# Kernel optimization log

Hardware: AMD Instinct MI355X
Metric: run time of the kernel (lower is better)

The kernel has to match this reference:

```python
import jax, jax.numpy as jnp
import numpy as np

D_MODEL = 1024
NHEAD = 16
D_HEAD = D_MODEL // NHEAD


def setup_inputs() -> dict:
    key = jax.random.key(0)
    ks = jax.random.split(key, 11)
    B, S = 4, 1024
    s = 1.0 / np.sqrt(D_MODEL)
    inp = {
        'q_in': jax.random.normal(ks[0], (B, S, D_MODEL), jnp.float32),
        'k_in': jax.random.normal(ks[1], (B, S, D_MODEL), jnp.float32),
        'v_in': jax.random.normal(ks[2], (B, S, D_MODEL), jnp.float32),
        'Wq': jax.random.normal(ks[3], (D_MODEL, D_MODEL), jnp.float32) * s,
        'bq': jnp.zeros((D_MODEL,), jnp.float32),
        'Wk': jax.random.normal(ks[4], (D_MODEL, D_MODEL), jnp.float32) * s,
        'bk': jnp.zeros((D_MODEL,), jnp.float32),
        'Wv': jax.random.normal(ks[5], (D_MODEL, D_MODEL), jnp.float32) * s,
        'bv': jnp.zeros((D_MODEL,), jnp.float32),
        'Wo': jax.random.normal(ks[6], (D_MODEL, D_MODEL), jnp.float32) * s,
        'bo': jnp.zeros((D_MODEL,), jnp.float32),
    }
    return inp


def reference(q_in, k_in, v_in, Wq, bq, Wk, bk, Wv, bv, Wo, bo):
    B, Sq, _ = q_in.shape
    Sk = k_in.shape[1]
    # Linear projections (torch Linear: x @ W.T + b; here W stored as [in, out])
    Q = q_in @ Wq + bq
    K = k_in @ Wk + bk
    V = v_in @ Wv + bv
    # [B, H, S, Dh]
    Qh = Q.reshape(B, Sq, NHEAD, D_HEAD).transpose(0, 2, 1, 3)
    Kh = K.reshape(B, Sk, NHEAD, D_HEAD).transpose(0, 2, 1, 3)
    Vh = V.reshape(B, Sk, NHEAD, D_HEAD).transpose(0, 2, 1, 3)
    scores = jnp.einsum('bhqd,bhkd->bhqk', Qh, Kh) / jnp.sqrt(jnp.float32(D_HEAD))
    attn_weights = jax.nn.softmax(scores, axis=-1)
    attn = jnp.einsum('bhqk,bhkd->bhqd', attn_weights, Vh)
    attn = attn.transpose(0, 2, 1, 3).reshape(B, Sq, D_MODEL)
    out = attn @ Wo + bo
    return out
```

## Files before the change

### kernel.cpp

```cpp
#include <hip/hip_runtime.h>
#include <hip/hip_bf16.h>
#include <cstdint>
#include <cstddef>

typedef __bf16 bf16_t;
typedef __bf16 bf16x8 __attribute__((ext_vector_type(8)));
typedef __bf16 bf16x4 __attribute__((ext_vector_type(4)));
typedef float f32x4 __attribute__((ext_vector_type(4)));

#define DM 1024
#define NHEAD 16
#define DHEAD 64

#define QSCALE 0.18033688011112042f
#define PSHIFT 4.0f
#define RS 72

__device__ __forceinline__ void gload_lds16(const void* g, void* l) {
    __builtin_amdgcn_global_load_lds(
        (const __attribute__((address_space(1))) void*)g,
        (__attribute__((address_space(3))) void*)l,
        16, 0, 0);
}

__device__ __forceinline__ uint4 cvt8(float4 lo, float4 hi) {
    union { bf16_t b[8]; uint4 u; } o;
    o.b[0] = (bf16_t)lo.x; o.b[1] = (bf16_t)lo.y; o.b[2] = (bf16_t)lo.z; o.b[3] = (bf16_t)lo.w;
    o.b[4] = (bf16_t)hi.x; o.b[5] = (bf16_t)hi.y; o.b[6] = (bf16_t)hi.z; o.b[7] = (bf16_t)hi.w;
    return o.u;
}

__global__ void prep(
    const float* __restrict__ q_in, const float* __restrict__ k_in, const float* __restrict__ v_in,
    bf16_t* __restrict__ Xq, bf16_t* __restrict__ Xk, bf16_t* __restrict__ Xv,
    const float* __restrict__ w0, const float* __restrict__ w1,
    const float* __restrict__ w2, const float* __restrict__ w3,
    bf16_t* __restrict__ t0, bf16_t* __restrict__ t1,
    bf16_t* __restrict__ t2, bf16_t* __restrict__ t3)
{
    __shared__ float tile[32][33];
    int id = blockIdx.x;
    if (id < 6144) {
        int plane = id >> 11;
        int blk = id & 2047;
        const float* x = plane == 0 ? q_in : plane == 1 ? k_in : v_in;
        bf16_t* y      = plane == 0 ? Xq   : plane == 1 ? Xk   : Xv;
        int i = (blk * 256 + threadIdx.x) * 8;
        float4 lo = *(const float4*)&x[i];
        float4 hi = *(const float4*)&x[i + 4];
        *(uint4*)&y[i] = cvt8(lo, hi);
    } else {
        int t = id - 6144;
        int zi = t >> 10;
        int blk = t & 1023;
        const float* w = zi == 0 ? w0 : zi == 1 ? w1 : zi == 2 ? w2 : w3;
        bf16_t* wt     = zi == 0 ? t0 : zi == 1 ? t1 : zi == 2 ? t2 : t3;
        int bx = (blk & 31) * 32;
        int by = (blk >> 5) * 32;
        int tx = threadIdx.x & 31, ty = threadIdx.x >> 5;
        for (int j = 0; j < 32; j += 8)
            tile[ty + j][tx] = w[(size_t)(by + ty + j) * DM + bx + tx];
        __syncthreads();
        for (int j = 0; j < 32; j += 8)
            wt[(size_t)(bx + ty + j) * DM + by + tx] = (bf16_t)tile[tx][ty + j];
    }
}

template <int MODE>
__device__ __forceinline__ void gemm_body(
    const bf16_t* __restrict__ A, const bf16_t* __restrict__ Bt,
    const float* __restrict__ bias, float scale,
    float* __restrict__ Cf, bf16_t* __restrict__ Cb,
    int r0, int c0, bf16_t* AsP, bf16_t* BsP)
{
    const int K = 1024;
    int tid  = threadIdx.x;
    int wave = tid >> 6;
    int lane = tid & 63;
    int quad = lane >> 4;
    int ln   = lane & 15;
    int wr   = wave >> 1;
    int wc   = wave & 1;

    f32x4 acc[4][4];
    for (int rb = 0; rb < 4; rb++)
        for (int cb = 0; cb < 4; cb++)
            acc[rb][cb] = (f32x4){0.f, 0.f, 0.f, 0.f};

    int sr = tid >> 2;
    int sk = (tid & 3) * 8;

    const bf16_t* gA0 = &A[(size_t)(r0 + sr) * K + sk];
    const bf16_t* gA1 = gA0 + (size_t)64 * K;
    const bf16_t* gB0 = &Bt[(size_t)(c0 + sr) * K + sk];
    const bf16_t* gB1 = gB0 + (size_t)64 * K;
    char* lA = (char*)AsP + wave * 1024;
    char* lB = (char*)BsP + wave * 1024;

    for (int k0 = 0; k0 < K; k0 += 32) {
        __syncthreads();
        gload_lds16(gA0 + k0, lA);
        gload_lds16(gA1 + k0, lA + 4096);
        gload_lds16(gB0 + k0, lB);
        gload_lds16(gB1 + k0, lB + 4096);
        __syncthreads();

        bf16x8 af[4], bfv[4];
        for (int rb = 0; rb < 4; rb++)
            af[rb] = *(const bf16x8*)&AsP[(wr * 64 + rb * 16 + ln) * 32 + quad * 8];
        for (int cb = 0; cb < 4; cb++)
            bfv[cb] = *(const bf16x8*)&BsP[(wc * 64 + cb * 16 + ln) * 32 + quad * 8];
        for (int rb = 0; rb < 4; rb++)
            for (int cb = 0; cb < 4; cb++)
                acc[rb][cb] = __builtin_amdgcn_mfma_f32_16x16x32_bf16(af[rb], bfv[cb], acc[rb][cb], 0, 0, 0);
    }

    for (int rb = 0; rb < 4; rb++) {
        for (int cb = 0; cb < 4; cb++) {
            int C = c0 + wc * 64 + cb * 16 + ln;
            for (int r = 0; r < 4; r++) {
                int R = r0 + wr * 64 + rb * 16 + quad * 4 + r;
                float v = acc[rb][cb][r];
                if (MODE == 0) {
                    Cf[(size_t)R * DM + C] = v + bias[C];
                } else if (MODE == 1) {
                    int b = R >> 10, s = R & 1023;
                    int h = C >> 6,  d = C & 63;
                    Cb[(((size_t)b * NHEAD + h) * 1024 + s) * DHEAD + d] =
                        (bf16_t)((v + bias[C]) * scale);
                } else {
                    Cb[((size_t)(C >> 10) * 1024 + R) * 1024 + (C & 1023)] =
                        (bf16_t)(v + bias[R]);
                }
            }
        }
    }
}

__global__ __launch_bounds__(256) void gemm_qkv(
    const bf16_t* __restrict__ Xq, const bf16_t* __restrict__ Xk, const bf16_t* __restrict__ Xv,
    const bf16_t* __restrict__ Wtq, const bf16_t* __restrict__ Wtk, const bf16_t* __restrict__ Wtv,
    const float* __restrict__ bq, const float* __restrict__ bk, const float* __restrict__ bv,
    bf16_t* __restrict__ Qd, bf16_t* __restrict__ Kd, bf16_t* __restrict__ Vt)
{
    __shared__ __align__(16) bf16_t As[128 * 32];
    __shared__ __align__(16) bf16_t Bs[128 * 32];
    int z = blockIdx.z;
    if (z == 0) {
        gemm_body<1>(Xq, Wtq, bq, QSCALE, nullptr, Qd,
                     blockIdx.x * 128, blockIdx.y * 128, As, Bs);
    } else if (z == 1) {
        gemm_body<1>(Xk, Wtk, bk, 1.0f, nullptr, Kd,
                     blockIdx.x * 128, blockIdx.y * 128, As, Bs);
    } else {
        gemm_body<2>(Wtv, Xv, bv, 1.0f, nullptr, Vt,
                     blockIdx.y * 128, blockIdx.x * 128, As, Bs);
    }
}

__global__ __launch_bounds__(256) void gemm_out(
    const bf16_t* __restrict__ At, const bf16_t* __restrict__ Wto,
    const float* __restrict__ bo, float* __restrict__ out)
{
    const int K = 1024;
    __shared__ __align__(16) bf16_t As[64 * 32];
    __shared__ __align__(16) bf16_t Bs[128 * 32];

    int tid  = threadIdx.x;
    int wave = tid >> 6;
    int lane = tid & 63;
    int quad = lane >> 4;
    int ln   = lane & 15;

    int r0 = blockIdx.x * 64;
    int c0 = blockIdx.y * 128;

    f32x4 acc[4][2];
    for (int rb = 0; rb < 4; rb++)
        for (int cb = 0; cb < 2; cb++)
            acc[rb][cb] = (f32x4){0.f, 0.f, 0.f, 0.f};

    int sr = tid >> 2;
    int sk = (tid & 3) * 8;

    const bf16_t* gA0 = At  + (size_t)(r0 + sr) * K + sk;
    const bf16_t* gB0 = Wto + (size_t)(c0 + sr) * K + sk;
    const bf16_t* gB1 = gB0 + (size_t)64 * K;
    char* lA = (char*)As + wave * 1024;
    char* lB = (char*)Bs + wave * 1024;

    for (int k0 = 0; k0 < K; k0 += 32) {
        __syncthreads();
        gload_lds16(gA0 + k0, lA);
        gload_lds16(gB0 + k0, lB);
        gload_lds16(gB1 + k0, lB + 4096);
        __syncthreads();

        bf16x8 af[4], bfv[2];
        for (int rb = 0; rb < 4; rb++)
            af[rb] = *(const bf16x8*)&As[(rb * 16 + ln) * 32 + quad * 8];
        for (int cb = 0; cb < 2; cb++)
            bfv[cb] = *(const bf16x8*)&Bs[(wave * 32 + cb * 16 + ln) * 32 + quad * 8];
        for (int rb = 0; rb < 4; rb++)
            for (int cb = 0; cb < 2; cb++)
                acc[rb][cb] = __builtin_amdgcn_mfma_f32_16x16x32_bf16(af[rb], bfv[cb], acc[rb][cb], 0, 0, 0);
    }

    for (int rb = 0; rb < 4; rb++) {
        for (int cb = 0; cb < 2; cb++) {
            int C = c0 + wave * 32 + cb * 16 + ln;
            float bn = bo[C];
            for (int r = 0; r < 4; r++) {
                int R = r0 + rb * 16 + quad * 4 + r;
                out[(size_t)R * DM + C] = acc[rb][cb][r] + bn;
            }
        }
    }
}

__global__ __launch_bounds__(256) void attn5(
    const bf16_t* __restrict__ Q,
    const bf16_t* __restrict__ K,
    const bf16_t* __restrict__ Vt,
    bf16_t* __restrict__ O)
{
    __shared__ __align__(16) bf16_t Ks[64 * RS];
    __shared__ __align__(16) bf16_t Vs[64 * RS];
    __shared__ __align__(16) bf16_t Ps[4][16 * RS];

    int tid  = threadIdx.x;
    int wave = tid >> 6;
    int lane = tid & 63;
    int quad = lane >> 4;
    int ln   = lane & 15;

    int bh = blockIdx.x;
    int q0w = blockIdx.y * 64 + wave * 16;

    const bf16_t* Qb = Q  + (size_t)bh * 65536;
    const bf16_t* Kb = K  + (size_t)bh * 65536;
    const bf16_t* Vb = Vt + (size_t)bh * 65536;

    int srow = tid >> 3;
    int scol = (tid & 7) * 8;
    const bf16_t* gK0 = Kb + (size_t)srow * 64 + scol;
    const bf16_t* gK1 = gK0 + 32 * 64;
    const bf16_t* gV0 = Vb + (size_t)srow * 1024 + scol;
    const bf16_t* gV1 = gV0 + 32 * 1024;

    bf16x8 aq0 = *(const bf16x8*)&Qb[(size_t)(q0w + ln) * 64 + quad * 8];
    bf16x8 aq1 = *(const bf16x8*)&Qb[(size_t)(q0w + ln) * 64 + 32 + quad * 8];

    uint4 rK0 = *(const uint4*)gK0;
    uint4 rK1 = *(const uint4*)gK1;
    uint4 rV0 = *(const uint4*)gV0;
    uint4 rV1 = *(const uint4*)gV1;

    float l_lane = 0.f;
    f32x4 o_acc[4];
    for (int cb = 0; cb < 4; cb++) o_acc[cb] = (f32x4){0.f, 0.f, 0.f, 0.f};

    bf16_t* Pw = Ps[wave];

    for (int kt = 0; kt < 16; kt++) {
        __syncthreads();
        *(uint4*)&Ks[srow * RS + scol]        = rK0;
        *(uint4*)&Ks[(32 + srow) * RS + scol] = rK1;
        *(uint4*)&Vs[srow * RS + scol]        = rV0;
        *(uint4*)&Vs[(32 + srow) * RS + scol] = rV1;
        __syncthreads();

        if (kt < 15) {
            gK0 += 4096; gK1 += 4096; gV0 += 64; gV1 += 64;
            rK0 = *(const uint4*)gK0;
            rK1 = *(const uint4*)gK1;
            rV0 = *(const uint4*)gV0;
            rV1 = *(const uint4*)gV1;
        }

        f32x4 sc[4];
        for (int kb = 0; kb < 4; kb++) {
            bf16x8 kf0 = *(const bf16x8*)&Ks[(kb * 16 + ln) * RS + quad * 8];
            bf16x8 kf1 = *(const bf16x8*)&Ks[(kb * 16 + ln) * RS + 32 + quad * 8];
            f32x4 a = (f32x4){0.f, 0.f, 0.f, 0.f};
            a = __builtin_amdgcn_mfma_f32_16x16x32_bf16(kf0, aq0, a, 0, 0, 0);
            a = __builtin_amdgcn_mfma_f32_16x16x32_bf16(kf1, aq1, a, 0, 0, 0);
            sc[kb] = a;
        }

        for (int kb = 0; kb < 4; kb++) {
            float p0 = __builtin_amdgcn_exp2f(sc[kb][0] - PSHIFT);
            float p1 = __builtin_amdgcn_exp2f(sc[kb][1] - PSHIFT);
            float p2 = __builtin_amdgcn_exp2f(sc[kb][2] - PSHIFT);
            float p3 = __builtin_amdgcn_exp2f(sc[kb][3] - PSHIFT);
            l_lane += (p0 + p1) + (p2 + p3);
            bf16x4 pk = (bf16x4){(bf16_t)p0, (bf16_t)p1, (bf16_t)p2, (bf16_t)p3};
            *(bf16x4*)&Pw[ln * RS + kb * 16 + quad * 4] = pk;
        }

        for (int kc = 0; kc < 2; kc++) {
            bf16x8 ap = *(const bf16x8*)&Pw[ln * RS + kc * 32 + quad * 8];
            for (int cb = 0; cb < 4; cb++) {
                bf16x8 vf = *(const bf16x8*)&Vs[(cb * 16 + ln) * RS + kc * 32 + quad * 8];
                o_acc[cb] = __builtin_amdgcn_mfma_f32_16x16x32_bf16(ap, vf, o_acc[cb], 0, 0, 0);
            }
        }
    }

    float l = l_lane;
    l += __shfl_xor(l, 16);
    l += __shfl_xor(l, 32);
    float invq[4];
    for (int r = 0; r < 4; r++)
        invq[r] = 1.f / __shfl(l, quad * 4 + r);

    int b = bh >> 4, h = bh & 15;
    for (int cb = 0; cb < 4; cb++) {
        for (int r = 0; r < 4; r++) {
            int q = q0w + quad * 4 + r;
            int d = cb * 16 + ln;
            O[((size_t)b * 1024 + q) * DM + h * 64 + d] = (bf16_t)(o_acc[cb][r] * invq[r]);
        }
    }
}

extern "C" void kernel_launch(void* const* d_in, const int* in_sizes, int n_in,
                              void* d_out, int out_size, void* d_ws, size_t ws_size,
                              hipStream_t stream) {
    const float* q_in = (const float*)d_in[0];
    const float* k_in = (const float*)d_in[1];
    const float* v_in = (const float*)d_in[2];
    const float* Wq   = (const float*)d_in[3];
    const float* bq   = (const float*)d_in[4];
    const float* Wk   = (const float*)d_in[5];
    const float* bk   = (const float*)d_in[6];
    const float* Wv   = (const float*)d_in[7];
    const float* bv   = (const float*)d_in[8];
    const float* Wo   = (const float*)d_in[9];
    const float* bo   = (const float*)d_in[10];

    char* ws = (char*)d_ws;
    const size_t MB = 1024ull * 1024ull;
    bf16_t* Xq  = (bf16_t*)(ws);
    bf16_t* Xk  = (bf16_t*)(ws + 8 * MB);
    bf16_t* Xv  = (bf16_t*)(ws + 16 * MB);
    bf16_t* Wtq = (bf16_t*)(ws + 24 * MB);
    bf16_t* Wtk = (bf16_t*)(ws + 26 * MB);
    bf16_t* Wtv = (bf16_t*)(ws + 28 * MB);
    bf16_t* Wto = (bf16_t*)(ws + 30 * MB);
    bf16_t* Qd  = (bf16_t*)(ws + 32 * MB);
    bf16_t* Kd  = (bf16_t*)(ws + 40 * MB);
    bf16_t* Vt  = (bf16_t*)(ws + 48 * MB);
    bf16_t* At  = Xq;

    prep<<<10240, 256, 0, stream>>>(q_in, k_in, v_in, Xq, Xk, Xv,
                                    Wq, Wk, Wv, Wo, Wtq, Wtk, Wtv, Wto);

    gemm_qkv<<<dim3(32, 8, 3), 256, 0, stream>>>(Xq, Xk, Xv,
                                                 Wtq, Wtk, Wtv, bq, bk, bv, Qd, Kd, Vt);

    attn5<<<dim3(64, 16), 256, 0, stream>>>(Qd, Kd, Vt, At);

    gemm_out<<<dim3(64, 8), 256, 0, stream>>>(At, Wto, bo, (float*)d_out);
}
```

Before: 214.6 us.

## Restructure attention to split keys across waves and reuse shared GEMM body for output

The attention kernel now has each wave own 16 keys of the 64-key tile and compute scores for all 64 queries. K and V tiles are loaded with direct global-to-LDS loads, P is shared through LDS, and row sums are reduced across waves at the end. This drops the register-staged K/V prefetch and per-wave redundant K reads, but adds a third barrier per tile and loses the overlap of the next tile's loads with compute. The output projection now reuses the 128x128 gemm_body tile instead of a dedicated 64x128 kernel, halving the grid.

```diff
diff --git a/kernel.cpp b/kernel.cpp
--- a/kernel.cpp
+++ b/kernel.cpp
@@ -162,162 +162,111 @@
     const bf16_t* __restrict__ At, const bf16_t* __restrict__ Wto,
     const float* __restrict__ bo, float* __restrict__ out)
 {
-    const int K = 1024;
-    __shared__ __align__(16) bf16_t As[64 * 32];
+    __shared__ __align__(16) bf16_t As[128 * 32];
     __shared__ __align__(16) bf16_t Bs[128 * 32];
-
-    int tid  = threadIdx.x;
-    int wave = tid >> 6;
-    int lane = tid & 63;
-    int quad = lane >> 4;
-    int ln   = lane & 15;
-
-    int r0 = blockIdx.x * 64;
-    int c0 = blockIdx.y * 128;
-
-    f32x4 acc[4][2];
-    for (int rb = 0; rb < 4; rb++)
-        for (int cb = 0; cb < 2; cb++)
-            acc[rb][cb] = (f32x4){0.f, 0.f, 0.f, 0.f};
-
-    int sr = tid >> 2;
-    int sk = (tid & 3) * 8;
-
-    const bf16_t* gA0 = At  + (size_t)(r0 + sr) * K + sk;
-    const bf16_t* gB0 = Wto + (size_t)(c0 + sr) * K + sk;
-    const bf16_t* gB1 = gB0 + (size_t)64 * K;
-    char* lA = (char*)As + wave * 1024;
-    char* lB = (char*)Bs + wave * 1024;
-
-    for (int k0 = 0; k0 < K; k0 += 32) {
-        __syncthreads();
-        gload_lds16(gA0 + k0, lA);
-        gload_lds16(gB0 + k0, lB);
-        gload_lds16(gB1 + k0, lB + 4096);
-        __syncthreads();
-
-        bf16x8 af[4], bfv[2];
-        for (int rb = 0; rb < 4; rb++)
-            af[rb] = *(const bf16x8*)&As[(rb * 16 + ln) * 32 + quad * 8];
-        for (int cb = 0; cb < 2; cb++)
-            bfv[cb] = *(const bf16x8*)&Bs[(wave * 32 + cb * 16 + ln) * 32 + quad * 8];
-        for (int rb = 0; rb < 4; rb++)
-            for (int cb = 0; cb < 2; cb++)
-                acc[rb][cb] = __builtin_amdgcn_mfma_f32_16x16x32_bf16(af[rb], bfv[cb], acc[rb][cb], 0, 0, 0);
-    }
-
-    for (int rb = 0; rb < 4; rb++) {
-        for (int cb = 0; cb < 2; cb++) {
-            int C = c0 + wave * 32 + cb * 16 + ln;
-            float bn = bo[C];
-            for (int r = 0; r < 4; r++) {
-                int R = r0 + rb * 16 + quad * 4 + r;
-                out[(size_t)R * DM + C] = acc[rb][cb][r] + bn;
-            }
-        }
-    }
-}
-
-__global__ __launch_bounds__(256) void attn5(
+    gemm_body<0>(At, Wto, bo, 1.0f, out, nullptr,
+                 blockIdx.x * 128, blockIdx.y * 128, As, Bs);
+}
+
+__global__ __launch_bounds__(256) void attn6(
     const bf16_t* __restrict__ Q,
     const bf16_t* __restrict__ K,
     const bf16_t* __restrict__ Vt,
     bf16_t* __restrict__ O)
 {
-    __shared__ __align__(16) bf16_t Ks[64 * RS];
-    __shared__ __align__(16) bf16_t Vs[64 * RS];
-    __shared__ __align__(16) bf16_t Ps[4][16 * RS];
+    __shared__ __align__(16) bf16_t Kp[2][64 * 32];
+    __shared__ __align__(16) bf16_t Vp[2][64 * 32];
+    __shared__ __align__(16) bf16_t Ps[64 * RS];
+    __shared__ float Ls[4][64];
 
     int tid  = threadIdx.x;
-    int wave = tid >> 6;
+    int w    = tid >> 6;
     int lane = tid & 63;
     int quad = lane >> 4;
     int ln   = lane & 15;
 
-    int bh = blockIdx.x;
-    int q0w = blockIdx.y * 64 + wave * 16;
+    int bh  = blockIdx.x;
+    int q0b = blockIdx.y * 64;
 
     const bf16_t* Qb = Q  + (size_t)bh * 65536;
     const bf16_t* Kb = K  + (size_t)bh * 65536;
     const bf16_t* Vb = Vt + (size_t)bh * 65536;
 
-    int srow = tid >> 3;
-    int scol = (tid & 7) * 8;
-    const bf16_t* gK0 = Kb + (size_t)srow * 64 + scol;
-    const bf16_t* gK1 = gK0 + 32 * 64;
-    const bf16_t* gV0 = Vb + (size_t)srow * 1024 + scol;
-    const bf16_t* gV1 = gV0 + 32 * 1024;
-
-    bf16x8 aq0 = *(const bf16x8*)&Qb[(size_t)(q0w + ln) * 64 + quad * 8];
-    bf16x8 aq1 = *(const bf16x8*)&Qb[(size_t)(q0w + ln) * 64 + 32 + quad * 8];
-
-    uint4 rK0 = *(const uint4*)gK0;
-    uint4 rK1 = *(const uint4*)gK1;
-    uint4 rV0 = *(const uint4*)gV0;
-    uint4 rV1 = *(const uint4*)gV1;
-
-    float l_lane = 0.f;
+    bf16x8 aq[4][2];
+    for (int st = 0; st < 4; st++)
+        for (int kc = 0; kc < 2; kc++)
+            aq[st][kc] = *(const bf16x8*)&Qb[(size_t)(q0b + st * 16 + ln) * 64 + kc * 32 + quad * 8];
+
+    int gr = w * 16 + (lane >> 2);
+    int gc = (lane & 3) * 8;
+    char* dK0 = (char*)&Kp[0][0] + w * 1024;
+    char* dK1 = (char*)&Kp[1][0] + w * 1024;
+    char* dV0 = (char*)&Vp[0][0] + w * 1024;
+    char* dV1 = (char*)&Vp[1][0] + w * 1024;
+    const bf16_t* srcV0 = Vb + (size_t)gr * 1024 + gc;
+    const bf16_t* srcV1 = srcV0 + 32;
+
+    float l_acc[4] = {0.f, 0.f, 0.f, 0.f};
     f32x4 o_acc[4];
     for (int cb = 0; cb < 4; cb++) o_acc[cb] = (f32x4){0.f, 0.f, 0.f, 0.f};
 
-    bf16_t* Pw = Ps[wave];
-
     for (int kt = 0; kt < 16; kt++) {
         __syncthreads();
-        *(uint4*)&Ks[srow * RS + scol]        = rK0;
-        *(uint4*)&Ks[(32 + srow) * RS + scol] = rK1;
-        *(uint4*)&Vs[srow * RS + scol]        = rV0;
-        *(uint4*)&Vs[(32 + srow) * RS + scol] = rV1;
-        __syncthreads();
-
-        if (kt < 15) {
-            gK0 += 4096; gK1 += 4096; gV0 += 64; gV1 += 64;
-            rK0 = *(const uint4*)gK0;
-            rK1 = *(const uint4*)gK1;
-            rV0 = *(const uint4*)gV0;
-            rV1 = *(const uint4*)gV1;
-        }
-
+        const bf16_t* kbase = Kb + (size_t)kt * 4096 + (size_t)gr * 64 + gc;
+        gload_lds16(kbase,          dK0);
+        gload_lds16(kbase + 32,     dK1);
+        gload_lds16(srcV0 + kt * 64, dV0);
+        gload_lds16(srcV1 + kt * 64, dV1);
+        __syncthreads();
+
+        bf16x8 kf0 = *(const bf16x8*)&Kp[0][(w * 16 + ln) * 32 + quad * 8];
+        bf16x8 kf1 = *(const bf16x8*)&Kp[1][(w * 16 + ln) * 32 + quad * 8];
         f32x4 sc[4];
-        for (int kb = 0; kb < 4; kb++) {
-            bf16x8 kf0 = *(const bf16x8*)&Ks[(kb * 16 + ln) * RS + quad * 8];
-            bf16x8 kf1 = *(const bf16x8*)&Ks[(kb * 16 + ln) * RS + 32 + quad * 8];
+        for (int st = 0; st < 4; st++) {
             f32x4 a = (f32x4){0.f, 0.f, 0.f, 0.f};
-            a = __builtin_amdgcn_mfma_f32_16x16x32_bf16(kf0, aq0, a, 0, 0, 0);
-            a = __builtin_amdgcn_mfma_f32_16x16x32_bf16(kf1, aq1, a, 0, 0, 0);
-            sc[kb] = a;
-        }
-
-        for (int kb = 0; kb < 4; kb++) {
-            float p0 = __builtin_amdgcn_exp2f(sc[kb][0] - PSHIFT);
-            float p1 = __builtin_amdgcn_exp2f(sc[kb][1] - PSHIFT);
-            float p2 = __builtin_amdgcn_exp2f(sc[kb][2] - PSHIFT);
-            float p3 = __builtin_amdgcn_exp2f(sc[kb][3] - PSHIFT);
-            l_lane += (p0 + p1) + (p2 + p3);
+            a = __builtin_amdgcn_mfma_f32_16x16x32_bf16(kf0, aq[st][0], a, 0, 0, 0);
+            a = __builtin_amdgcn_mfma_f32_16x16x32_bf16(kf1, aq[st][1], a, 0, 0, 0);
+            sc[st] = a;
+        }
+
+        for (int st = 0; st < 4; st++) {
+            float p0 = __builtin_amdgcn_exp2f(sc[st][0] - PSHIFT);
+            float p1 = __builtin_amdgcn_exp2f(sc[st][1] - PSHIFT);
+            float p2 = __builtin_amdgcn_exp2f(sc[st][2] - PSHIFT);
+            float p3 = __builtin_amdgcn_exp2f(sc[st][3] - PSHIFT);
+            l_acc[st] += (p0 + p1) + (p2 + p3);
             bf16x4 pk = (bf16x4){(bf16_t)p0, (bf16_t)p1, (bf16_t)p2, (bf16_t)p3};
-            *(bf16x4*)&Pw[ln * RS + kb * 16 + quad * 4] = pk;
-        }
-
-        for (int kc = 0; kc < 2; kc++) {
-            bf16x8 ap = *(const bf16x8*)&Pw[ln * RS + kc * 32 + quad * 8];
-            for (int cb = 0; cb < 4; cb++) {
-                bf16x8 vf = *(const bf16x8*)&Vs[(cb * 16 + ln) * RS + kc * 32 + quad * 8];
-                o_acc[cb] = __builtin_amdgcn_mfma_f32_16x16x32_bf16(ap, vf, o_acc[cb], 0, 0, 0);
-            }
-        }
-    }
-
-    float l = l_lane;
-    l += __shfl_xor(l, 16);
-    l += __shfl_xor(l, 32);
+            *(bf16x4*)&Ps[(st * 16 + ln) * RS + w * 16 + quad * 4] = pk;
+        }
+        __syncthreads();
+
+        bf16x8 ap0 = *(const bf16x8*)&Ps[(w * 16 + ln) * RS + quad * 8];
+        bf16x8 ap1 = *(const bf16x8*)&Ps[(w * 16 + ln) * RS + 32 + quad * 8];
+        for (int cb = 0; cb < 4; cb++) {
+            bf16x8 vf0 = *(const bf16x8*)&Vp[0][(cb * 16 + ln) * 32 + quad * 8];
+            o_acc[cb] = __builtin_amdgcn_mfma_f32_16x16x32_bf16(ap0, vf0, o_acc[cb], 0, 0, 0);
+            bf16x8 vf1 = *(const bf16x8*)&Vp[1][(cb * 16 + ln) * 32 + quad * 8];
+            o_acc[cb] = __builtin_amdgcn_mfma_f32_16x16x32_bf16(ap1, vf1, o_acc[cb], 0, 0, 0);
+        }
+    }
+
+    for (int st = 0; st < 4; st++) {
+        float ls = l_acc[st];
+        ls += __shfl_xor(ls, 16);
+        ls += __shfl_xor(ls, 32);
+        if (lane < 16) Ls[w][st * 16 + lane] = ls;
+    }
+    __syncthreads();
+    float lt = Ls[0][w * 16 + ln] + Ls[1][w * 16 + ln]
+             + Ls[2][w * 16 + ln] + Ls[3][w * 16 + ln];
     float invq[4];
     for (int r = 0; r < 4; r++)
-        invq[r] = 1.f / __shfl(l, quad * 4 + r);
+        invq[r] = 1.f / __shfl(lt, quad * 4 + r);
 
     int b = bh >> 4, h = bh & 15;
     for (int cb = 0; cb < 4; cb++) {
         for (int r = 0; r < 4; r++) {
-            int q = q0w + quad * 4 + r;
+            int q = q0b + w * 16 + quad * 4 + r;
             int d = cb * 16 + ln;
             O[((size_t)b * 1024 + q) * DM + h * 64 + d] = (bf16_t)(o_acc[cb][r] * invq[r]);
         }
@@ -359,7 +308,7 @@
     gemm_qkv<<<dim3(32, 8, 3), 256, 0, stream>>>(Xq, Xk, Xv,
                                                  Wtq, Wtk, Wtv, bq, bk, bv, Qd, Kd, Vt);
 
-    attn5<<<dim3(64, 16), 256, 0, stream>>>(Qd, Kd, Vt, At);
-
-    gemm_out<<<dim3(64, 8), 256, 0, stream>>>(At, Wto, bo, (float*)d_out);
-}
+    attn6<<<dim3(64, 16), 256, 0, stream>>>(Qd, Kd, Vt, At);
+
+    gemm_out<<<dim3(32, 8), 256, 0, stream>>>(At, Wto, bo, (float*)d_out);
+}
```

Result: slower. 252.1 us (+17.5%).
